# Performance work log

Measured on AMD Instinct MI355X. Metric: run time of the kernel, lower is better.

Reference implementation:

```python
import jax, jax.numpy as jnp
import numpy as np
from jax import lax

SIGMOID_THRESH = 0.05  # hard-coded in get_local_max_coords
KERNEL = 3             # default kernel_size


def setup_inputs() -> dict:
    key = jax.random.key(0)
    # [B, num_kps, H, W] heatmap logits from the DeepLab head
    heatmaps = jax.random.normal(key, (16, 17, 384, 384), dtype=jnp.float32)
    return {"heatmaps": heatmaps}


def reference(heatmaps):
    """CenterNet-style local-max peak extraction.

    Faithful to Heatmaps.get_local_max_coords: a pixel is a peak iff it equals
    the 3x3 max-pool of the logits AND sigmoid(logit) > 0.05. Instead of the
    data-dependent torch.nonzero + Python grouping loops (which just reshuffle
    the same information into ragged per-image/per-type lists), we return the
    dense, fixed-shape peak-score map: sigmoid(logit) at peak locations, 0
    elsewhere. The [B, K, H, W] layout already encodes the per-image (axis 0)
    and per-keypoint-type (axis 1) grouping of the original nested loops.
    """
    # 3x3 max-pool, stride 1, SAME padding (pad = kernel // 2)
    max_hm = lax.reduce_window(
        heatmaps,
        -jnp.inf,
        lax.max,
        window_dimensions=(1, 1, KERNEL, KERNEL),
        window_strides=(1, 1, 1, 1),
        padding="SAME",
    )
    prob = jax.nn.sigmoid(heatmaps)
    peak_mask = (max_hm == heatmaps) & (prob > SIGMOID_THRESH)
    return jnp.where(peak_mask, prob, jnp.zeros((), dtype=heatmaps.dtype))
```

## Files before the change

### kernel.cpp

```cpp
#include <hip/hip_runtime.h>
#include <math.h>

#define HH 384
#define WW 384
#define NIMG 272
#define IMG_STRIDE (HH * WW)
#define ROWS 8
#define NROWLD (ROWS + 2)
#define STRIPS (HH / ROWS)
#define C4N (WW / 4)
#define BLOCK 256
#define NBLOCKS (NIMG * STRIPS * C4N / BLOCK)
#define NXCD 8

typedef float f4_t __attribute__((ext_vector_type(4)));

__device__ __forceinline__ float max3f(float a, float b, float c) {
    return fmaxf(fmaxf(a, b), c);
}
__device__ __forceinline__ float fast_sigmoid(float v) {
    return __fdividef(1.0f, 1.0f + __expf(-v));
}

__global__ __launch_bounds__(BLOCK) void
heatmap_peaks_batch(const float* __restrict__ in, float* __restrict__ out) {
    const float NEG = -INFINITY;
    const f4_t NEG4 = {NEG, NEG, NEG, NEG};

    int bid = blockIdx.x;
    int swz = (bid % NXCD) * (NBLOCKS / NXCD) + bid / NXCD;

    int u   = swz * BLOCK + (int)threadIdx.x;
    int c4  = u % C4N;
    int t   = u / C4N;
    int s   = t % STRIPS;
    int img = t / STRIPS;
    int y0  = s * ROWS;

    const float* ib = in  + (size_t)img * IMG_STRIDE + c4 * 4;
    float*       ob = out + (size_t)img * IMG_STRIDE + (size_t)y0 * WW + c4 * 4;

    const bool has_l = (c4 > 0);
    const bool has_r = (c4 < C4N - 1);
    const int  loff  = has_l ? -1 : 0;
    const int  roff  = has_r ?  4 : 3;

    f4_t v[NROWLD]; float l[NROWLD], r[NROWLD];
#pragma unroll
    for (int k = 0; k < NROWLD; ++k) {
        int gy = y0 - 1 + k;
        int cy = gy < 0 ? 0 : (gy > HH - 1 ? HH - 1 : gy);
        const float* p = ib + (size_t)cy * WW;
        v[k] = *(const f4_t*)p;
        l[k] = p[loff];
        r[k] = p[roff];
    }

#pragma unroll
    for (int k = 0; k < NROWLD; ++k) {
        if (!has_l) l[k] = NEG;
        if (!has_r) r[k] = NEG;
    }
    if (y0 == 0)            { v[0] = NEG4;          l[0] = NEG;          r[0] = NEG; }
    if (y0 + ROWS == HH)    { v[NROWLD-1] = NEG4;   l[NROWLD-1] = NEG;   r[NROWLD-1] = NEG; }

    f4_t h[NROWLD];
#pragma unroll
    for (int k = 0; k < NROWLD; ++k) {
        h[k].x = max3f(l[k],   v[k].x, v[k].y);
        h[k].y = max3f(v[k].x, v[k].y, v[k].z);
        h[k].z = max3f(v[k].y, v[k].z, v[k].w);
        h[k].w = max3f(v[k].z, v[k].w, r[k]);
    }

#pragma unroll
    for (int j = 0; j < ROWS; ++j) {
        f4_t c = v[j + 1];
        f4_t o; float m, p;
        m = max3f(h[j].x, h[j+1].x, h[j+2].x); p = fast_sigmoid(c.x);
        o.x = (m == c.x && p > 0.05f) ? p : 0.0f;
        m = max3f(h[j].y, h[j+1].y, h[j+2].y); p = fast_sigmoid(c.y);
        o.y = (m == c.y && p > 0.05f) ? p : 0.0f;
        m = max3f(h[j].z, h[j+1].z, h[j+2].z); p = fast_sigmoid(c.z);
        o.z = (m == c.z && p > 0.05f) ? p : 0.0f;
        m = max3f(h[j].w, h[j+1].w, h[j+2].w); p = fast_sigmoid(c.w);
        o.w = (m == c.w && p > 0.05f) ? p : 0.0f;
        __builtin_nontemporal_store(o, (f4_t*)(ob + (size_t)j * WW));
    }
}

extern "C" void kernel_launch(void* const* d_in, const int* in_sizes, int n_in,
                              void* d_out, int out_size, void* d_ws, size_t ws_size,
                              hipStream_t stream) {
    const float* in = (const float*)d_in[0];
    float* out = (float*)d_out;
    heatmap_peaks_batch<<<NBLOCKS, BLOCK, 0, stream>>>(in, out);
}
```

Baseline: 275.9 us.

## Stage 64x64 tiles with halo in LDS and compute per-column from shared memory

Replaces the register-only 8-row strip kernel with a 2D-tiled kernel that loads a 66x72 haloed tile into shared memory via float4 loads, then each thread computes 16 rows of one column from LDS. The aim is to cut redundant halo reads (the old kernel re-read 2 of every 10 rows plus scalar left/right neighbours) and the uncoalesced scalar edge loads. In exchange it adds an LDS round-trip, a barrier, and scalar (non-vector) nontemporal stores, and the halo overhead per 64x64 tile is still about 16%.

```diff
diff --git a/kernel.cpp b/kernel.cpp
--- a/kernel.cpp
+++ b/kernel.cpp
@@ -5,13 +5,17 @@
 #define WW 384
 #define NIMG 272
 #define IMG_STRIDE (HH * WW)
-#define ROWS 8
-#define NROWLD (ROWS + 2)
-#define STRIPS (HH / ROWS)
-#define C4N (WW / 4)
-#define BLOCK 256
-#define NBLOCKS (NIMG * STRIPS * C4N / BLOCK)
+#define TW 64
+#define TH 64
+#define TX 6
+#define TY 6
+#define NBLOCKS (TX * TY * NIMG)
 #define NXCD 8
+#define LDS_W 72
+#define LDS_H 66
+#define ROW_F4 18
+#define NL4 (LDS_H * ROW_F4)
+#define NLD 5
 
 typedef float f4_t __attribute__((ext_vector_type(4)));
 
@@ -22,70 +26,75 @@
     return __fdividef(1.0f, 1.0f + __expf(-v));
 }
 
-__global__ __launch_bounds__(BLOCK) void
-heatmap_peaks_batch(const float* __restrict__ in, float* __restrict__ out) {
+__global__ __launch_bounds__(256, 4) void
+heatmap_peaks_tile(const float* __restrict__ in, float* __restrict__ out) {
+    __shared__ float S[LDS_H * LDS_W];
     const float NEG = -INFINITY;
     const f4_t NEG4 = {NEG, NEG, NEG, NEG};
 
-    int bid = blockIdx.x;
+    int tid = (int)threadIdx.x;
+    int bid = (int)blockIdx.x;
     int swz = (bid % NXCD) * (NBLOCKS / NXCD) + bid / NXCD;
 
-    int u   = swz * BLOCK + (int)threadIdx.x;
-    int c4  = u % C4N;
-    int t   = u / C4N;
-    int s   = t % STRIPS;
-    int img = t / STRIPS;
-    int y0  = s * ROWS;
+    int txt = swz % TX;
+    int tmp = swz / TX;
+    int tyt = tmp % TY;
+    int img = tmp / TY;
+    int x0  = txt * TW;
+    int y0  = tyt * TH;
 
-    const float* ib = in  + (size_t)img * IMG_STRIDE + c4 * 4;
-    float*       ob = out + (size_t)img * IMG_STRIDE + (size_t)y0 * WW + c4 * 4;
+    const float* ib = in + (size_t)img * IMG_STRIDE;
 
-    const bool has_l = (c4 > 0);
-    const bool has_r = (c4 < C4N - 1);
-    const int  loff  = has_l ? -1 : 0;
-    const int  roff  = has_r ?  4 : 3;
+    f4_t va[NLD];
+    int  la[NLD];
+    bool act[NLD];
+#pragma unroll
+    for (int k = 0; k < NLD; ++k) {
+        int e   = tid + k * 256;
+        int row = e / ROW_F4;
+        int c4  = e - row * ROW_F4;
+        int gy  = y0 - 1 + row;
+        int gx  = x0 - 4 + c4 * 4;
+        bool vy = (unsigned)gy < (unsigned)HH;
+        bool vx = (unsigned)gx <= (unsigned)(WW - 4);
+        bool inr = (e < NL4);
+        int cy = vy ? gy : 0;
+        int cx = vx ? gx : 0;
+        f4_t v = *(const f4_t*)(ib + (size_t)cy * WW + cx);
+        va[k]  = (vx && vy && inr) ? v : NEG4;
+        la[k]  = row * LDS_W + c4 * 4;
+        act[k] = inr;
+    }
+#pragma unroll
+    for (int k = 0; k < NLD; ++k)
+        if (act[k]) *(f4_t*)&S[la[k]] = va[k];
+    __syncthreads();
 
-    f4_t v[NROWLD]; float l[NROWLD], r[NROWLD];
+    int c  = tid & 63;
+    int q  = tid >> 6;
+    int lc = 4 + c;
+    int rbase = q * 16;
+
+    float h[18], val[18];
 #pragma unroll
-    for (int k = 0; k < NROWLD; ++k) {
-        int gy = y0 - 1 + k;
-        int cy = gy < 0 ? 0 : (gy > HH - 1 ? HH - 1 : gy);
-        const float* p = ib + (size_t)cy * WW;
-        v[k] = *(const f4_t*)p;
-        l[k] = p[loff];
-        r[k] = p[roff];
+    for (int j = 0; j < 18; ++j) {
+        const float* row = &S[(rbase + j) * LDS_W + lc];
+        float l = row[-1];
+        float m = row[0];
+        float r = row[1];
+        h[j]   = max3f(l, m, r);
+        val[j] = m;
     }
 
+    float* ob = out + (size_t)img * IMG_STRIDE
+                    + (size_t)(y0 + rbase) * WW + x0 + c;
 #pragma unroll
-    for (int k = 0; k < NROWLD; ++k) {
-        if (!has_l) l[k] = NEG;
-        if (!has_r) r[k] = NEG;
-    }
-    if (y0 == 0)            { v[0] = NEG4;          l[0] = NEG;          r[0] = NEG; }
-    if (y0 + ROWS == HH)    { v[NROWLD-1] = NEG4;   l[NROWLD-1] = NEG;   r[NROWLD-1] = NEG; }
-
-    f4_t h[NROWLD];
-#pragma unroll
-    for (int k = 0; k < NROWLD; ++k) {
-        h[k].x = max3f(l[k],   v[k].x, v[k].y);
-        h[k].y = max3f(v[k].x, v[k].y, v[k].z);
-        h[k].z = max3f(v[k].y, v[k].z, v[k].w);
-        h[k].w = max3f(v[k].z, v[k].w, r[k]);
-    }
-
-#pragma unroll
-    for (int j = 0; j < ROWS; ++j) {
-        f4_t c = v[j + 1];
-        f4_t o; float m, p;
-        m = max3f(h[j].x, h[j+1].x, h[j+2].x); p = fast_sigmoid(c.x);
-        o.x = (m == c.x && p > 0.05f) ? p : 0.0f;
-        m = max3f(h[j].y, h[j+1].y, h[j+2].y); p = fast_sigmoid(c.y);
-        o.y = (m == c.y && p > 0.05f) ? p : 0.0f;
-        m = max3f(h[j].z, h[j+1].z, h[j+2].z); p = fast_sigmoid(c.z);
-        o.z = (m == c.z && p > 0.05f) ? p : 0.0f;
-        m = max3f(h[j].w, h[j+1].w, h[j+2].w); p = fast_sigmoid(c.w);
-        o.w = (m == c.w && p > 0.05f) ? p : 0.0f;
-        __builtin_nontemporal_store(o, (f4_t*)(ob + (size_t)j * WW));
+    for (int j = 0; j < 16; ++j) {
+        float m = max3f(h[j], h[j + 1], h[j + 2]);
+        float v = val[j + 1];
+        float p = fast_sigmoid(v);
+        float o = (m == v && p > 0.05f) ? p : 0.0f;
+        __builtin_nontemporal_store(o, ob + (size_t)j * WW);
     }
 }
 
@@ -94,5 +103,5 @@
                               hipStream_t stream) {
     const float* in = (const float*)d_in[0];
     float* out = (float*)d_out;
-    heatmap_peaks_batch<<<NBLOCKS, BLOCK, 0, stream>>>(in, out);
+    heatmap_peaks_tile<<<NBLOCKS, 256, 0, stream>>>(in, out);
 }
```

New measurement: 273.0 us. About the same (-1.1%).

## Roll 32-row column segments with double-buffered loads and shuffle-based halos

Applied to the files above, without the earlier changes.

Each 32-lane group now walks a 128-wide, 32-row segment, streaming rows in double-buffered groups of four and carrying horizontal-max rows between steps. This cuts the vertical halo overhead from 10/8 to 34/32 loads. Horizontal neighbours come from warp shuffles instead of per-thread scalar side loads, and only the edge lanes fetch halo columns. The cost is fewer resident threads with more registers each, and a longer serial dependency chain per thread.

```diff
diff --git a/kernel.cpp b/kernel.cpp
--- a/kernel.cpp
+++ b/kernel.cpp
@@ -5,12 +5,14 @@
 #define WW 384
 #define NIMG 272
 #define IMG_STRIDE (HH * WW)
-#define ROWS 8
-#define NROWLD (ROWS + 2)
-#define STRIPS (HH / ROWS)
-#define C4N (WW / 4)
-#define BLOCK 256
-#define NBLOCKS (NIMG * STRIPS * C4N / BLOCK)
+#define BWD 128
+#define XB 3
+#define SEG 32
+#define YS (HH / SEG)
+#define UPI (XB * YS)
+#define UNITS (NIMG * UPI)
+#define GPB 8
+#define NBLOCKS (UNITS / GPB)
 #define NXCD 8
 
 typedef float f4_t __attribute__((ext_vector_type(4)));
@@ -22,71 +24,123 @@
     return __fdividef(1.0f, 1.0f + __expf(-v));
 }
 
-__global__ __launch_bounds__(BLOCK) void
-heatmap_peaks_batch(const float* __restrict__ in, float* __restrict__ out) {
+__global__ __launch_bounds__(256, 4) void
+heatmap_peaks_roll(const float* __restrict__ in, float* __restrict__ out) {
     const float NEG = -INFINITY;
     const f4_t NEG4 = {NEG, NEG, NEG, NEG};
 
-    int bid = blockIdx.x;
+    int tid = (int)threadIdx.x;
+    int f4c = tid & 31;
+    int grp = tid >> 5;
+    int bid = (int)blockIdx.x;
     int swz = (bid % NXCD) * (NBLOCKS / NXCD) + bid / NXCD;
+    int u   = swz * GPB + grp;
+    int img = u / UPI;
+    int rem = u % UPI;
+    int ys  = rem % YS;
+    int xb  = rem / YS;
+    int x0  = xb * BWD;
+    int y0  = ys * SEG;
 
-    int u   = swz * BLOCK + (int)threadIdx.x;
-    int c4  = u % C4N;
-    int t   = u / C4N;
-    int s   = t % STRIPS;
-    int img = t / STRIPS;
-    int y0  = s * ROWS;
+    const float* ib = in + (size_t)img * IMG_STRIDE;
+    int xc = x0 + 4 * f4c;
+    const float* cb = ib + xc;
 
-    const float* ib = in  + (size_t)img * IMG_STRIDE + c4 * 4;
-    float*       ob = out + (size_t)img * IMG_STRIDE + (size_t)y0 * WW + c4 * 4;
+    const bool eL = (f4c == 0), eR = (f4c == 31);
+    const bool has_l = (x0 > 0), has_r = (x0 + BWD < WW);
+    int ex = eR ? (has_r ? x0 + BWD : WW - 1) : (has_l ? x0 - 1 : 0);
+    const float* eb = ib + ex;
+    const bool edge = (eL && has_l) || (eR && has_r);
 
-    const bool has_l = (c4 > 0);
-    const bool has_r = (c4 < C4N - 1);
-    const int  loff  = has_l ? -1 : 0;
-    const int  roff  = has_r ?  4 : 3;
+    auto LD4 = [&](int ry0, f4_t* Bv, float* Ev) {
+#pragma unroll
+        for (int r2 = 0; r2 < 4; ++r2) {
+            int gy = y0 + ry0 + r2;
+            gy = gy < 0 ? 0 : (gy > HH - 1 ? HH - 1 : gy);
+            Bv[r2] = *(const f4_t*)(cb + (size_t)gy * WW);
+            if (edge) Ev[r2] = eb[(size_t)gy * WW];
+        }
+    };
+    auto HM = [&](f4_t b, float e) -> f4_t {
+        float lw = __shfl_up(b.w, 1, 32);
+        float rx = __shfl_down(b.x, 1, 32);
+        float L = eL ? (has_l ? e : NEG) : lw;
+        float R = eR ? (has_r ? e : NEG) : rx;
+        f4_t h;
+        h.x = max3f(L,   b.x, b.y);
+        h.y = max3f(b.x, b.y, b.z);
+        h.z = max3f(b.y, b.z, b.w);
+        h.w = max3f(b.z, b.w, R);
+        return h;
+    };
 
-    f4_t v[NROWLD]; float l[NROWLD], r[NROWLD];
-#pragma unroll
-    for (int k = 0; k < NROWLD; ++k) {
-        int gy = y0 - 1 + k;
-        int cy = gy < 0 ? 0 : (gy > HH - 1 ? HH - 1 : gy);
-        const float* p = ib + (size_t)cy * WW;
-        v[k] = *(const f4_t*)p;
-        l[k] = p[loff];
-        r[k] = p[roff];
+    float* ob = out + (size_t)img * IMG_STRIDE + (size_t)y0 * WW + xc;
+    auto EMIT = [&](int oy, f4_t v, f4_t a, f4_t b, f4_t c) {
+        f4_t o; float m, p;
+        m = max3f(a.x, b.x, c.x); p = fast_sigmoid(v.x);
+        o.x = (m == v.x && p > 0.05f) ? p : 0.0f;
+        m = max3f(a.y, b.y, c.y); p = fast_sigmoid(v.y);
+        o.y = (m == v.y && p > 0.05f) ? p : 0.0f;
+        m = max3f(a.z, b.z, c.z); p = fast_sigmoid(v.z);
+        o.z = (m == v.z && p > 0.05f) ? p : 0.0f;
+        m = max3f(a.w, b.w, c.w); p = fast_sigmoid(v.w);
+        o.w = (m == v.w && p > 0.05f) ? p : 0.0f;
+        __builtin_nontemporal_store(o, (f4_t*)(ob + (size_t)oy * WW));
+    };
+
+    f4_t A[4], B[4];
+    float EA[4] = {NEG, NEG, NEG, NEG}, EB[4] = {NEG, NEG, NEG, NEG};
+    f4_t hc0, hc1, vc;
+
+#define CONSUME(C, EC, r0) do {                                   \
+        f4_t hn0 = HM(C[0], EC[0]);                               \
+        f4_t hn1 = HM(C[1], EC[1]);                               \
+        f4_t hn2 = HM(C[2], EC[2]);                               \
+        f4_t hn3 = HM(C[3], EC[3]);                               \
+        EMIT((r0) - 1, vc,   hc0, hc1, hn0);                      \
+        EMIT((r0),     C[0], hc1, hn0, hn1);                      \
+        EMIT((r0) + 1, C[1], hn0, hn1, hn2);                      \
+        EMIT((r0) + 2, C[2], hn1, hn2, hn3);                      \
+        hc0 = hn2; hc1 = hn3; vc = C[3];                          \
+    } while (0)
+
+    LD4(-1, A, EA);
+    LD4( 3, B, EB);
+    {
+        f4_t h0 = HM(A[0], EA[0]);
+        if (y0 == 0) h0 = NEG4;
+        f4_t h1 = HM(A[1], EA[1]);
+        f4_t h2 = HM(A[2], EA[2]);
+        f4_t h3 = HM(A[3], EA[3]);
+        EMIT(0, A[1], h0, h1, h2);
+        EMIT(1, A[2], h1, h2, h3);
+        hc0 = h2; hc1 = h3; vc = A[3];
     }
-
-#pragma unroll
-    for (int k = 0; k < NROWLD; ++k) {
-        if (!has_l) l[k] = NEG;
-        if (!has_r) r[k] = NEG;
+    LD4( 7, A, EA); CONSUME(B, EB,  3);
+    LD4(11, B, EB); CONSUME(A, EA,  7);
+    LD4(15, A, EA); CONSUME(B, EB, 11);
+    LD4(19, B, EB); CONSUME(A, EA, 15);
+    LD4(23, A, EA); CONSUME(B, EB, 19);
+    LD4(27, B, EB); CONSUME(A, EA, 23);
+    f4_t EV0, EV1; float EE0 = NEG, EE1 = NEG;
+    {
+        int gy = y0 + 31;
+        EV0 = *(const f4_t*)(cb + (size_t)gy * WW);
+        if (edge) EE0 = eb[(size_t)gy * WW];
+        int gz = y0 + 32;
+        gz = gz > HH - 1 ? HH - 1 : gz;
+        EV1 = *(const f4_t*)(cb + (size_t)gz * WW);
+        if (edge) EE1 = eb[(size_t)gz * WW];
     }
-    if (y0 == 0)            { v[0] = NEG4;          l[0] = NEG;          r[0] = NEG; }
-    if (y0 + ROWS == HH)    { v[NROWLD-1] = NEG4;   l[NROWLD-1] = NEG;   r[NROWLD-1] = NEG; }
-
-    f4_t h[NROWLD];
-#pragma unroll
-    for (int k = 0; k < NROWLD; ++k) {
-        h[k].x = max3f(l[k],   v[k].x, v[k].y);
-        h[k].y = max3f(v[k].x, v[k].y, v[k].z);
-        h[k].z = max3f(v[k].y, v[k].z, v[k].w);
-        h[k].w = max3f(v[k].z, v[k].w, r[k]);
+    CONSUME(B, EB, 27);
+    {
+        f4_t hE0 = HM(EV0, EE0);
+        f4_t hE1 = HM(EV1, EE1);
+        if (ys == YS - 1) hE1 = NEG4;
+        EMIT(30, vc,  hc0, hc1, hE0);
+        EMIT(31, EV0, hc1, hE0, hE1);
     }
-
-#pragma unroll
-    for (int j = 0; j < ROWS; ++j) {
-        f4_t c = v[j + 1];
-        f4_t o; float m, p;
-        m = max3f(h[j].x, h[j+1].x, h[j+2].x); p = fast_sigmoid(c.x);
-        o.x = (m == c.x && p > 0.05f) ? p : 0.0f;
-        m = max3f(h[j].y, h[j+1].y, h[j+2].y); p = fast_sigmoid(c.y);
-        o.y = (m == c.y && p > 0.05f) ? p : 0.0f;
-        m = max3f(h[j].z, h[j+1].z, h[j+2].z); p = fast_sigmoid(c.z);
-        o.z = (m == c.z && p > 0.05f) ? p : 0.0f;
-        m = max3f(h[j].w, h[j+1].w, h[j+2].w); p = fast_sigmoid(c.w);
-        o.w = (m == c.w && p > 0.05f) ? p : 0.0f;
-        __builtin_nontemporal_store(o, (f4_t*)(ob + (size_t)j * WW));
-    }
+#undef CONSUME
 }
 
 extern "C" void kernel_launch(void* const* d_in, const int* in_sizes, int n_in,
@@ -94,5 +148,5 @@
                               hipStream_t stream) {
     const float* in = (const float*)d_in[0];
     float* out = (float*)d_out;
-    heatmap_peaks_batch<<<NBLOCKS, BLOCK, 0, stream>>>(in, out);
+    heatmap_peaks_roll<<<NBLOCKS, 256, 0, stream>>>(in, out);
 }
```

After: 281.1 us. Within noise of the previous version (+1.9%).
